# Optimization experiments

Hardware: AMD Instinct MI355X
Metric: run time of the kernel (lower is better)

The kernel has to match this reference:

```python
import jax, jax.numpy as jnp
import numpy as np

B, S, D = 8, 1024, 1152
H, HD = 16, 72  # num_heads, head_dim

def setup_inputs() -> dict:
    key = jax.random.key(0)
    ks = jax.random.split(key, 7)
    hidden_states = jax.random.normal(ks[0], (B, S, D), dtype=jnp.float32)
    cos = jax.random.uniform(ks[1], (S, HD), dtype=jnp.float32)
    sin = jax.random.uniform(ks[2], (S, HD), dtype=jnp.float32)
    qkv_w = jax.random.normal(ks[3], (3 * D, D), dtype=jnp.float32) * 0.02
    qkv_b = jnp.zeros((3 * D,), dtype=jnp.float32)
    proj_w = jax.random.normal(ks[4], (D, D), dtype=jnp.float32) * 0.02
    proj_b = jnp.zeros((D,), dtype=jnp.float32)
    return {"hidden_states": hidden_states, "cos": cos, "sin": sin,
            "qkv_w": qkv_w, "qkv_b": qkv_b, "proj_w": proj_w, "proj_b": proj_b}

def _rotate_half(x):
    x1, x2 = jnp.split(x, 2, axis=-1)
    return jnp.concatenate((-x2, x1), axis=-1)

def reference(hidden_states, cos, sin, qkv_w, qkv_b, proj_w, proj_b):
    b, s, d = hidden_states.shape
    # fused QKV projection
    qkv = hidden_states @ qkv_w.T + qkv_b            # [B,S,3D]
    qkv = qkv.reshape(b, s, 3, H, HD)
    qkv = jnp.transpose(qkv, (2, 0, 3, 1, 4))        # [3,B,H,S,HD]
    q, k, v = qkv[0], qkv[1], qkv[2]
    # rotary embedding, cos/sin broadcast [1,1,S,HD]
    c = cos[None, None, :, :]
    sn = sin[None, None, :, :]
    q = q * c + _rotate_half(q) * sn
    k = k * c + _rotate_half(k) * sn
    # SDPA
    scale = HD ** -0.5
    scores = jnp.einsum('bhqd,bhkd->bhqk', q, k) * scale
    probs = jax.nn.softmax(scores, axis=-1)
    attn = jnp.einsum('bhqk,bhkd->bhqd', probs, v)   # [B,H,S,HD]
    attn = jnp.transpose(attn, (0, 2, 1, 3)).reshape(b, s, d)
    return attn @ proj_w.T + proj_b
```

## Files before the change

kernel.cpp:

```cpp
#include <hip/hip_runtime.h>
#include <hip/hip_bf16.h>


typedef __attribute__((ext_vector_type(8))) short short8;
typedef __attribute__((ext_vector_type(4))) float f32x4;

__device__ __forceinline__ unsigned int f2bf(float f) {
    unsigned int u = __float_as_uint(f);
    return (u + 0x7FFFu + ((u >> 16) & 1u)) >> 16;
}
__device__ __forceinline__ float bf2f(unsigned short u) {
    return __uint_as_float((unsigned int)u << 16);
}

__device__ __forceinline__ void stout(float* C, size_t idx, float v) { C[idx] = v; }
__device__ __forceinline__ void stout(__hip_bfloat16* C, size_t idx, float v) {
    C[idx] = __float2bfloat16(v);
}

__device__ __forceinline__ void async_cp16(const void* g, void* l) {
    __builtin_amdgcn_global_load_lds((const __attribute__((address_space(1))) void*)g,
                                     (__attribute__((address_space(3))) void*)l, 16, 0, 0);
}

__global__ void f32_to_bf16_pair(
    const float* __restrict__ s0, unsigned short* __restrict__ d0, int n0_4,
    const float* __restrict__ s1, unsigned short* __restrict__ d1, int n1_4,
    unsigned short* __restrict__ dz, int nz_4)
{
    int i = blockIdx.x * 256 + threadIdx.x;
    if (i < n0_4) {
        float4 f = ((const float4*)s0)[i];
        ushort4 r;
        r.x = (unsigned short)f2bf(f.x);
        r.y = (unsigned short)f2bf(f.y);
        r.z = (unsigned short)f2bf(f.z);
        r.w = (unsigned short)f2bf(f.w);
        ((ushort4*)d0)[i] = r;
        return;
    }
    i -= n0_4;
    if (i < n1_4) {
        float4 f = ((const float4*)s1)[i];
        ushort4 r;
        r.x = (unsigned short)f2bf(f.x);
        r.y = (unsigned short)f2bf(f.y);
        r.z = (unsigned short)f2bf(f.z);
        r.w = (unsigned short)f2bf(f.w);
        ((ushort4*)d1)[i] = r;
        return;
    }
    i -= n1_4;
    if (i < nz_4) {
        ushort4 z; z.x = 0; z.y = 0; z.z = 0; z.w = 0;
        ((ushort4*)dz)[i] = z;
    }
}

template <int ISB, int H>
__device__ __forceinline__ void stage_ht(const unsigned short* __restrict__ g, int ldg,
                                         int k0, unsigned short* l, int w, int lane)
{
#pragma unroll
    for (int t = 0; t < 2; t++) {
        const int c  = w * 2 + t;
        const int r0 = ISB ? ((c >> 2) * 64 + H * 32 + (c & 3) * 8)
                           : ((c & 8) * 16 + H * 64 + (c & 7) * 8);
        const int rl = r0 + (lane >> 3);
        const int gg = (lane & 7) ^ (lane >> 3);
        async_cp16(g + (size_t)rl * ldg + k0 + gg * 8, l + r0 * 64);
    }
}

#define LDA(MH, SRC)                                                              \
    _Pragma("unroll") for (int mi = 0; mi < 4; ++mi) {                            \
        Af[mi][0] = *(const short8*)((SRC) + aRow + (MH) * 4096 + mi * 1024 + g0); \
        Af[mi][1] = *(const short8*)((SRC) + aRow + (MH) * 4096 + mi * 1024 + g1); \
    }

#define LDB(DST, NH, SRC)                                                         \
    _Pragma("unroll") for (int ni = 0; ni < 2; ++ni) {                            \
        DST[ni][0] = *(const short8*)((SRC) + bRow + (NH) * 2048 + ni * 1024 + g0); \
        DST[ni][1] = *(const short8*)((SRC) + bRow + (NH) * 2048 + ni * 1024 + g1); \
    }

#define MFMAS(MH, NH, PB)                                                         \
    __builtin_amdgcn_s_setprio(1);                                                \
    _Pragma("unroll") for (int mi = 0; mi < 4; ++mi)                              \
    _Pragma("unroll") for (int ni = 0; ni < 2; ++ni) {                            \
        acc[(MH) * 4 + mi][(NH) * 2 + ni] = __builtin_amdgcn_mfma_f32_16x16x32_bf16( \
            Af[mi][0], PB[ni][0], acc[(MH) * 4 + mi][(NH) * 2 + ni], 0, 0, 0);    \
        acc[(MH) * 4 + mi][(NH) * 2 + ni] = __builtin_amdgcn_mfma_f32_16x16x32_bf16( \
            Af[mi][1], PB[ni][1], acc[(MH) * 4 + mi][(NH) * 2 + ni], 0, 0, 0);    \
    }                                                                             \
    __builtin_amdgcn_s_setprio(0);

#define MIDBAR()                                                   \
    do {                                                           \
        __builtin_amdgcn_s_barrier();                              \
        asm volatile("s_waitcnt lgkmcnt(0)" ::: "memory");         \
        __builtin_amdgcn_sched_barrier(0);                         \
    } while (0)

#define ENDBAR()                                                   \
    do {                                                           \
        __builtin_amdgcn_s_barrier();                              \
        __builtin_amdgcn_sched_barrier(0);                         \
    } while (0)

template <typename OT>
__global__ __launch_bounds__(512, 2) void gemm_bt_256(
    const __hip_bfloat16* __restrict__ Abf,
    const __hip_bfloat16* __restrict__ Bbf,
    const float* __restrict__ bias,
    OT* __restrict__ C,
    int M, int Nreal, int K)
{
    __shared__ __align__(16) unsigned short smem[2][2][256 * 64];

    const int tid  = threadIdx.x;
    const int lane = tid & 63;
    const int w    = tid >> 6;
    const int wm   = w >> 2;
    const int wn   = w & 3;
    const int q    = lane >> 4;
    const int fr   = lane & 15;
    const int xr   = fr & 7;

    const int nwg = gridDim.x * gridDim.y;
    const int lin = blockIdx.y * gridDim.x + blockIdx.x;
    const int swz = (lin & 7) * (nwg >> 3) + (lin >> 3);
    const int bn  = (swz % gridDim.x) * 256;
    const int bm  = (swz / gridDim.x) * 256;

    const unsigned short* Ag = (const unsigned short*)Abf + (size_t)bm * K;
    const unsigned short* Bg = (const unsigned short*)Bbf + (size_t)bn * K;

    unsigned short* s00 = &smem[0][0][0];
    unsigned short* s01 = &smem[0][1][0];
    unsigned short* s10 = &smem[1][0][0];
    unsigned short* s11 = &smem[1][1][0];

    const int NT = K >> 6;
    const int NI = NT >> 1;

    const int aRow = (wm * 128 + fr) * 64;
    const int bRow = (wn * 64 + fr) * 64;
    const int g0   = ((0 * 4 + q) ^ xr) * 8;
    const int g1   = ((1 * 4 + q) ^ xr) * 8;

    f32x4 acc[8][4];
#pragma unroll
    for (int i = 0; i < 8; i++)
#pragma unroll
        for (int j = 0; j < 4; j++) acc[i][j] = (f32x4){0.f, 0.f, 0.f, 0.f};

    short8 Af[4][2], Bf0[2][2], Bf1[2][2];

    stage_ht<0, 0>(Ag, K, 0, s00, w, lane);
    stage_ht<0, 1>(Ag, K, 0, s00, w, lane);
    stage_ht<1, 0>(Bg, K, 0, s01, w, lane);
    stage_ht<1, 1>(Bg, K, 0, s01, w, lane);
    stage_ht<0, 0>(Ag, K, 64, s10, w, lane);
    stage_ht<1, 1>(Bg, K, 64, s10 + 16384, w, lane);
    stage_ht<0, 1>(Ag, K, 64, s10, w, lane);
    asm volatile("s_waitcnt vmcnt(6)" ::: "memory");
    ENDBAR();

#pragma unroll 1
    for (int i = 0; i < NI; i++) {
        const int k1 = (2 * i + 1) * 64;
        const int t2 = 2 * i + 2, t3 = 2 * i + 3;
        const int k2 = (t2 < NT ? t2 : NT - 1) * 64;
        const int k3 = (t3 < NT ? t3 : NT - 1) * 64;

        LDA(0, s00);
        LDB(Bf0, 0, s01);
        stage_ht<1, 0>(Bg, K, k1, s11, w, lane);
        asm volatile("s_waitcnt lgkmcnt(8)" ::: "memory");
        MIDBAR();
        MFMAS(0, 0, Bf0);
        ENDBAR();

        LDB(Bf1, 1, s01);
        stage_ht<0, 0>(Ag, K, k2, s00, w, lane);
        MIDBAR();
        MFMAS(0, 1, Bf1);
        ENDBAR();

        LDA(1, s00);
        stage_ht<1, 1>(Bg, K, k2, s01, w, lane);
        MIDBAR();
        MFMAS(1, 1, Bf1);
        ENDBAR();

        stage_ht<0, 1>(Ag, K, k2, s00, w, lane);
        asm volatile("s_waitcnt vmcnt(6)" ::: "memory");
        MIDBAR();
        MFMAS(1, 0, Bf0);
        ENDBAR();

        LDA(0, s10);
        LDB(Bf0, 0, s11);
        stage_ht<1, 0>(Bg, K, k2, s01, w, lane);
        asm volatile("s_waitcnt lgkmcnt(8)" ::: "memory");
        MIDBAR();
        MFMAS(0, 0, Bf0);
        ENDBAR();

        LDB(Bf1, 1, s11);
        stage_ht<0, 0>(Ag, K, k3, s10, w, lane);
        MIDBAR();
        MFMAS(0, 1, Bf1);
        ENDBAR();

        LDA(1, s10);
        stage_ht<1, 1>(Bg, K, k3, s11, w, lane);
        MIDBAR();
        MFMAS(1, 1, Bf1);
        ENDBAR();

        stage_ht<0, 1>(Ag, K, k3, s10, w, lane);
        asm volatile("s_waitcnt vmcnt(6)" ::: "memory");
        MIDBAR();
        MFMAS(1, 0, Bf0);
        ENDBAR();
    }

#pragma unroll
    for (int mf = 0; mf < 8; mf++) {
        const int row = bm + wm * 128 + mf * 16 + q * 4;
#pragma unroll
        for (int nf = 0; nf < 4; nf++) {
            const int col = bn + wn * 64 + nf * 16 + fr;
            if (col < Nreal) {
                const float bv = bias[col];
#pragma unroll
                for (int r = 0; r < 4; r++)
                    stout(C, (size_t)(row + r) * Nreal + col, acc[mf][nf][r] + bv);
            }
        }
    }
}

__global__ void rope_v_prep(
    const __hip_bfloat16* __restrict__ qkv,
    const float* __restrict__ cosp,
    const float* __restrict__ sinp,
    __hip_bfloat16* __restrict__ Qo,
    __hip_bfloat16* __restrict__ Ko,
    __hip_bfloat16* __restrict__ Vt)
{
    __shared__ __align__(16) unsigned short T[64 * 72];
    const int tid = threadIdx.x;
    const int bh = blockIdx.x >> 4;
    const int st = blockIdx.x & 15;
    const int b = bh >> 4, h = bh & 15;
    const size_t row0 = ((size_t)b * 1024 + st * 64) * 3456;

    const unsigned short* vsrc = (const unsigned short*)qkv + row0 + 2304 + h * 72;
#pragma unroll
    for (int k = 0; k < 3; k++) {
        const int c = tid + k * 256;
        if (c < 576) {
            const int s = c / 9, off = (c % 9) * 8;
            *(uint4*)&T[c * 8] = *(const uint4*)(vsrc + (size_t)s * 3456 + off);
        }
    }

    const unsigned short* qkvp = (const unsigned short*)qkv;
    const float QS = 0.17002324f;
#pragma unroll
    for (int k = 0; k < 3; k++) {
        const int idx = tid + k * 256;
        if (idx < 576) {
            const int sl = idx / 9, iq = idx % 9;
            const int i0 = iq * 4;
            const int sg = st * 64 + sl;
            const unsigned short* qrow = qkvp + row0 + (size_t)sl * 3456 + h * 72 + i0;

            ushort4 ql = *(const ushort4*)(qrow);
            ushort4 qh = *(const ushort4*)(qrow + 36);
            ushort4 kl = *(const ushort4*)(qrow + 1152);
            ushort4 kh = *(const ushort4*)(qrow + 1188);
            float4 cl = *(const float4*)(cosp + sg * 72 + i0);
            float4 ch = *(const float4*)(cosp + sg * 72 + i0 + 36);
            float4 nl = *(const float4*)(sinp + sg * 72 + i0);
            float4 nh = *(const float4*)(sinp + sg * 72 + i0 + 36);

            unsigned short qlv[4] = {ql.x, ql.y, ql.z, ql.w};
            unsigned short qhv[4] = {qh.x, qh.y, qh.z, qh.w};
            unsigned short klv[4] = {kl.x, kl.y, kl.z, kl.w};
            unsigned short khv[4] = {kh.x, kh.y, kh.z, kh.w};
            float clv[4] = {cl.x, cl.y, cl.z, cl.w};
            float chv[4] = {ch.x, ch.y, ch.z, ch.w};
            float nlv[4] = {nl.x, nl.y, nl.z, nl.w};
            float nhv[4] = {nh.x, nh.y, nh.z, nh.w};

            unsigned short qol[4], qoh[4], kol[4], koh[4];
#pragma unroll
            for (int j = 0; j < 4; j++) {
                const float qa = bf2f(qlv[j]), qb = bf2f(qhv[j]);
                const float ka = bf2f(klv[j]), kb = bf2f(khv[j]);
                qol[j] = (unsigned short)f2bf((qa * clv[j] - qb * nlv[j]) * QS);
                qoh[j] = (unsigned short)f2bf((qb * chv[j] + qa * nhv[j]) * QS);
                kol[j] = (unsigned short)f2bf(ka * clv[j] - kb * nlv[j]);
                koh[j] = (unsigned short)f2bf(kb * chv[j] + ka * nhv[j]);
            }
            unsigned short* qob = (unsigned short*)Qo + ((size_t)bh * 1024 + sg) * 72 + i0;
            unsigned short* kob = (unsigned short*)Ko + ((size_t)bh * 1024 + sg) * 80 + i0;
            *(ushort4*)qob        = (ushort4){qol[0], qol[1], qol[2], qol[3]};
            *(ushort4*)(qob + 36) = (ushort4){qoh[0], qoh[1], qoh[2], qoh[3]};
            *(ushort4*)kob        = (ushort4){kol[0], kol[1], kol[2], kol[3]};
            *(ushort4*)(kob + 36) = (ushort4){koh[0], koh[1], koh[2], koh[3]};
        }
    }

    __syncthreads();

    unsigned short* dst = (unsigned short*)Vt + (size_t)(bh * 16 + st) * 80 * 64;
#pragma unroll
    for (int k = 0; k < 9; k++) {
        const int o = tid + k * 256;
        const int d = o >> 5;
        const int sl = (o & 31) * 2;
        ushort2 v;
        v.x = T[sl * 72 + d];
        v.y = T[(sl + 1) * 72 + d];
        *(ushort2*)&dst[d * 64 + sl] = v;
    }
    if (tid < 64) dst[72 * 64 + tid] = (unsigned short)0x3F80;
    for (int z = tid; z < 7 * 64; z += 256) dst[73 * 64 + z] = 0;
}

__global__ __launch_bounds__(256, 4) void attn_mfma(
    const __hip_bfloat16* __restrict__ Q,
    const __hip_bfloat16* __restrict__ K,
    const __hip_bfloat16* __restrict__ Vt,
    __hip_bfloat16* __restrict__ O)
{
    __shared__ __align__(16) unsigned short Ps[4][32][72];

    const int tid  = threadIdx.x;
    const int lane = tid & 63;
    const int w    = tid >> 6;
    const int quad = lane >> 4;
    const int fr   = lane & 15;
    const int bh   = blockIdx.x & 127;
    const int qt   = blockIdx.x >> 7;
    const int qbase = qt * 128 + w * 32;

    const short8 z8 = (short8){0,0,0,0,0,0,0,0};

    const unsigned short* qp = (const unsigned short*)Q + ((size_t)bh * 1024 + qbase + fr) * 72;
    short8 qf[2][3];
#pragma unroll
    for (int sub = 0; sub < 2; sub++) {
        const unsigned short* qs = qp + sub * 16 * 72;
        qf[sub][0] = *(const short8*)(qs + quad * 8);
        qf[sub][1] = *(const short8*)(qs + 32 + quad * 8);
        qf[sub][2] = (quad == 0) ? *(const short8*)(qs + 64) : z8;
    }

    f32x4 Oa[2][5];
#pragma unroll
    for (int sub = 0; sub < 2; sub++)
#pragma unroll
        for (int n = 0; n < 5; n++) Oa[sub][n] = (f32x4){0.f, 0.f, 0.f, 0.f};

    const unsigned short* kg0 = (const unsigned short*)K + (size_t)bh * 1024 * 80;
    const unsigned short* vg0 = (const unsigned short*)Vt + (size_t)bh * 16 * 80 * 64;

#pragma unroll 1
    for (int t = 0; t < 16; t++) {
        const unsigned short* kg = kg0 + (size_t)t * 64 * 80;
        const unsigned short* vg = vg0 + (size_t)t * 80 * 64;

#pragma unroll
        for (int nt = 0; nt < 4; nt++) {
            const unsigned short* kr = kg + (nt * 16 + fr) * 80;
            short8 b0 = *(const short8*)(kr + quad * 8);
            short8 b1 = *(const short8*)(kr + 32 + quad * 8);
            short8 b2 = (quad == 0) ? *(const short8*)(kr + 64) : z8;
            f32x4 s0 = (f32x4){0.f, 0.f, 0.f, 0.f};
            f32x4 s1 = (f32x4){0.f, 0.f, 0.f, 0.f};
            __builtin_amdgcn_s_setprio(1);
            s0 = __builtin_amdgcn_mfma_f32_16x16x32_bf16(qf[0][0], b0, s0, 0, 0, 0);
            s1 = __builtin_amdgcn_mfma_f32_16x16x32_bf16(qf[1][0], b0, s1, 0, 0, 0);
            s0 = __builtin_amdgcn_mfma_f32_16x16x32_bf16(qf[0][1], b1, s0, 0, 0, 0);
            s1 = __builtin_amdgcn_mfma_f32_16x16x32_bf16(qf[1][1], b1, s1, 0, 0, 0);
            s0 = __builtin_amdgcn_mfma_f32_16x16x32_bf16(qf[0][2], b2, s0, 0, 0, 0);
            s1 = __builtin_amdgcn_mfma_f32_16x16x32_bf16(qf[1][2], b2, s1, 0, 0, 0);
            __builtin_amdgcn_s_setprio(0);
#pragma unroll
            for (int r = 0; r < 4; r++) {
                Ps[w][quad * 4 + r][nt * 16 + fr]      = (unsigned short)f2bf(exp2f(s0[r]));
                Ps[w][16 + quad * 4 + r][nt * 16 + fr] = (unsigned short)f2bf(exp2f(s1[r]));
            }
        }

#pragma unroll
        for (int ks = 0; ks < 2; ks++) {
            short8 ap0 = *(const short8*)&Ps[w][fr][ks * 32 + quad * 8];
            short8 ap1 = *(const short8*)&Ps[w][16 + fr][ks * 32 + quad * 8];
            short8 bv[5];
#pragma unroll
            for (int n = 0; n < 5; n++)
                bv[n] = *(const short8*)(vg + (n * 16 + fr) * 64 + ks * 32 + quad * 8);
            __builtin_amdgcn_s_setprio(1);
#pragma unroll
            for (int n = 0; n < 5; n++) {
                Oa[0][n] = __builtin_amdgcn_mfma_f32_16x16x32_bf16(ap0, bv[n], Oa[0][n], 0, 0, 0);
                Oa[1][n] = __builtin_amdgcn_mfma_f32_16x16x32_bf16(ap1, bv[n], Oa[1][n], 0, 0, 0);
            }
            __builtin_amdgcn_s_setprio(0);
        }
    }

    const int lsrc = (lane & 48) | 8;
    const int b = bh >> 4, h = bh & 15;
    unsigned short* ob = (unsigned short*)O;
#pragma unroll
    for (int sub = 0; sub < 2; sub++) {
        float inv[4];
#pragma unroll
        for (int r = 0; r < 4; r++)
            inv[r] = 1.f / __shfl(Oa[sub][4][r], lsrc, 64);
#pragma unroll
        for (int n = 0; n < 5; n++) {
            const int d = n * 16 + fr;
            if (d < 72) {
#pragma unroll
                for (int r = 0; r < 4; r++) {
                    const size_t idx =
                        ((size_t)b * 1024 + qbase + sub * 16 + quad * 4 + r) * 1152 + h * 72 + d;
                    ob[idx] = (unsigned short)f2bf(Oa[sub][n][r] * inv[r]);
                }
            }
        }
    }
}

extern "C" void kernel_launch(void* const* d_in, const int* in_sizes, int n_in,
                              void* d_out, int out_size, void* d_ws, size_t ws_size,
                              hipStream_t stream)
{
    const float* hs     = (const float*)d_in[0];
    const float* cosp   = (const float*)d_in[1];
    const float* sinp   = (const float*)d_in[2];
    const float* qkv_w  = (const float*)d_in[3];
    const float* qkv_b  = (const float*)d_in[4];
    const float* proj_w = (const float*)d_in[5];
    const float* proj_b = (const float*)d_in[6];
    float* out = (float*)d_out;

    char* ws = (char*)d_ws;
    __hip_bfloat16* qkv_buf = (__hip_bfloat16*)ws;
    __hip_bfloat16* Qb = (__hip_bfloat16*)(ws + 56623104);
    __hip_bfloat16* Kb = Qb + 9437184;
    __hip_bfloat16* Vt = Kb + 10485760;
    __hip_bfloat16* Ab = qkv_buf;

    unsigned short* hs_bf = (unsigned short*)Qb;
    unsigned short* qw_bf = (unsigned short*)Kb;
    unsigned short* pw_bf = (unsigned short*)Qb;

    f32_to_bf16_pair<<<13248, 256, 0, stream>>>(hs, hs_bf, 2359296,
                                                qkv_w, qw_bf, 995328,
                                                qw_bf + 3981312, 36864);
    gemm_bt_256<__hip_bfloat16>
        <<<dim3(14, 32), 512, 0, stream>>>((const __hip_bfloat16*)hs_bf,
                                           (const __hip_bfloat16*)qw_bf,
                                           qkv_b, qkv_buf, 8192, 3456, 1152);
    rope_v_prep<<<2048, 256, 0, stream>>>(qkv_buf, cosp, sinp, Qb, Kb, Vt);
    attn_mfma<<<1024, 256, 0, stream>>>(Qb, Kb, Vt, Ab);
    f32_to_bf16_pair<<<1440, 256, 0, stream>>>(proj_w, pw_bf, 331776,
                                               nullptr, nullptr, 0,
                                               pw_bf + 1327104, 36864);
    gemm_bt_256<float>
        <<<dim3(5, 32), 512, 0, stream>>>((const __hip_bfloat16*)Ab,
                                          (const __hip_bfloat16*)pw_bf,
                                          proj_b, out, 8192, 1152, 1152);
}
```

Before: 348.1 us.

## Stage K/V tiles in LDS with register-prefetched double buffering in attention

The attention kernel now cooperatively loads each 64-key K tile and V^T tile into shared memory, prefetching the next tile into registers while computing the current one, instead of every wave reading K/V straight from global memory. K and V^T are stored with a 72-element stride rather than padded to 80. The ones row and zero padding for V that produce the softmax denominator are now written once into LDS instead of global memory. This trades redundant global/L2 traffic across the four waves for two block-wide barriers per tile and extra LDS use, which may reduce occupancy.

After: 344.4 us. About the same (-1.1%).

```diff
diff --git a/kernel.cpp b/kernel.cpp
--- a/kernel.cpp
+++ b/kernel.cpp
@@ -308,7 +308,7 @@
                 koh[j] = (unsigned short)f2bf(kb * chv[j] + ka * nhv[j]);
             }
             unsigned short* qob = (unsigned short*)Qo + ((size_t)bh * 1024 + sg) * 72 + i0;
-            unsigned short* kob = (unsigned short*)Ko + ((size_t)bh * 1024 + sg) * 80 + i0;
+            unsigned short* kob = (unsigned short*)Ko + ((size_t)bh * 1024 + sg) * 72 + i0;
             *(ushort4*)qob        = (ushort4){qol[0], qol[1], qol[2], qol[3]};
             *(ushort4*)(qob + 36) = (ushort4){qoh[0], qoh[1], qoh[2], qoh[3]};
             *(ushort4*)kob        = (ushort4){kol[0], kol[1], kol[2], kol[3]};
@@ -318,7 +318,7 @@
 
     __syncthreads();
 
-    unsigned short* dst = (unsigned short*)Vt + (size_t)(bh * 16 + st) * 80 * 64;
+    unsigned short* dst = (unsigned short*)Vt + (size_t)(bh * 16 + st) * 72 * 64;
 #pragma unroll
     for (int k = 0; k < 9; k++) {
         const int o = tid + k * 256;
@@ -329,8 +329,6 @@
         v.y = T[(sl + 1) * 72 + d];
         *(ushort2*)&dst[d * 64 + sl] = v;
     }
-    if (tid < 64) dst[72 * 64 + tid] = (unsigned short)0x3F80;
-    for (int z = tid; z < 7 * 64; z += 256) dst[73 * 64 + z] = 0;
 }
 
 __global__ __launch_bounds__(256, 4) void attn_mfma(
@@ -339,6 +337,8 @@
     const __hip_bfloat16* __restrict__ Vt,
     __hip_bfloat16* __restrict__ O)
 {
+    __shared__ __align__(16) unsigned short Ks[64 * 72];
+    __shared__ __align__(16) unsigned short Vs[80][72];
     __shared__ __align__(16) unsigned short Ps[4][32][72];
 
     const int tid  = threadIdx.x;
@@ -352,6 +352,9 @@
 
     const short8 z8 = (short8){0,0,0,0,0,0,0,0};
 
+    for (int idx = tid; idx < 8 * 72; idx += 256)
+        Vs[72 + idx / 72][idx % 72] = (idx < 72) ? (unsigned short)0x3F80 : (unsigned short)0;
+
     const unsigned short* qp = (const unsigned short*)Q + ((size_t)bh * 1024 + qbase + fr) * 72;
     short8 qf[2][3];
 #pragma unroll
@@ -368,17 +371,46 @@
 #pragma unroll
         for (int n = 0; n < 5; n++) Oa[sub][n] = (f32x4){0.f, 0.f, 0.f, 0.f};
 
-    const unsigned short* kg0 = (const unsigned short*)K + (size_t)bh * 1024 * 80;
-    const unsigned short* vg0 = (const unsigned short*)Vt + (size_t)bh * 16 * 80 * 64;
+    const unsigned short* kg0 = (const unsigned short*)K + (size_t)bh * 1024 * 72;
+    const unsigned short* vg0 = (const unsigned short*)Vt + (size_t)bh * 16 * 72 * 64;
+
+    const unsigned short* gsrc[5];
+    unsigned short* ldst[5];
+#pragma unroll
+    for (int c = 0; c < 5; c++) {
+        const int g = tid + c * 256;
+        if (g < 576) {
+            gsrc[c] = kg0 + g * 8;
+            ldst[c] = &Ks[g * 8];
+        } else {
+            const int v = (g - 576) & 1023;
+            gsrc[c] = vg0 + (size_t)v * 8;
+            ldst[c] = &Vs[v >> 3][(v & 7) * 8];
+        }
+    }
+    const bool five = (tid < 128);
+
+    uint4 stg[5];
+#pragma unroll
+    for (int c = 0; c < 4; c++) stg[c] = *(const uint4*)(gsrc[c]);
+    if (five) stg[4] = *(const uint4*)(gsrc[4]);
+#pragma unroll
+    for (int c = 0; c < 4; c++) *(uint4*)ldst[c] = stg[c];
+    if (five) *(uint4*)ldst[4] = stg[4];
+    __syncthreads();
 
 #pragma unroll 1
     for (int t = 0; t < 16; t++) {
-        const unsigned short* kg = kg0 + (size_t)t * 64 * 80;
-        const unsigned short* vg = vg0 + (size_t)t * 80 * 64;
+        if (t < 15) {
+            const size_t off = (size_t)(t + 1) * 4608;
+#pragma unroll
+            for (int c = 0; c < 4; c++) stg[c] = *(const uint4*)(gsrc[c] + off);
+            if (five) stg[4] = *(const uint4*)(gsrc[4] + off);
+        }
 
 #pragma unroll
         for (int nt = 0; nt < 4; nt++) {
-            const unsigned short* kr = kg + (nt * 16 + fr) * 80;
+            const unsigned short* kr = &Ks[(nt * 16 + fr) * 72];
             short8 b0 = *(const short8*)(kr + quad * 8);
             short8 b1 = *(const short8*)(kr + 32 + quad * 8);
             short8 b2 = (quad == 0) ? *(const short8*)(kr + 64) : z8;
@@ -403,17 +435,22 @@
         for (int ks = 0; ks < 2; ks++) {
             short8 ap0 = *(const short8*)&Ps[w][fr][ks * 32 + quad * 8];
             short8 ap1 = *(const short8*)&Ps[w][16 + fr][ks * 32 + quad * 8];
-            short8 bv[5];
-#pragma unroll
-            for (int n = 0; n < 5; n++)
-                bv[n] = *(const short8*)(vg + (n * 16 + fr) * 64 + ks * 32 + quad * 8);
-            __builtin_amdgcn_s_setprio(1);
 #pragma unroll
             for (int n = 0; n < 5; n++) {
-                Oa[0][n] = __builtin_amdgcn_mfma_f32_16x16x32_bf16(ap0, bv[n], Oa[0][n], 0, 0, 0);
-                Oa[1][n] = __builtin_amdgcn_mfma_f32_16x16x32_bf16(ap1, bv[n], Oa[1][n], 0, 0, 0);
+                short8 bv = *(const short8*)&Vs[n * 16 + fr][ks * 32 + quad * 8];
+                __builtin_amdgcn_s_setprio(1);
+                Oa[0][n] = __builtin_amdgcn_mfma_f32_16x16x32_bf16(ap0, bv, Oa[0][n], 0, 0, 0);
+                Oa[1][n] = __builtin_amdgcn_mfma_f32_16x16x32_bf16(ap1, bv, Oa[1][n], 0, 0, 0);
+                __builtin_amdgcn_s_setprio(0);
             }
-            __builtin_amdgcn_s_setprio(0);
+        }
+
+        if (t < 15) {
+            __syncthreads();
+#pragma unroll
+            for (int c = 0; c < 4; c++) *(uint4*)ldst[c] = stg[c];
+            if (five) *(uint4*)ldst[4] = stg[4];
+            __syncthreads();
         }
     }
 
@@ -458,7 +495,7 @@
     __hip_bfloat16* qkv_buf = (__hip_bfloat16*)ws;
     __hip_bfloat16* Qb = (__hip_bfloat16*)(ws + 56623104);
     __hip_bfloat16* Kb = Qb + 9437184;
-    __hip_bfloat16* Vt = Kb + 10485760;
+    __hip_bfloat16* Vt = Kb + 9437184;
     __hip_bfloat16* Ab = qkv_buf;
 
     unsigned short* hs_bf = (unsigned short*)Qb;
```

## Stage K/V tiles in LDS with double-buffered async copies in attention

Applied to the files above, without the earlier changes.

The attention kernel now copies each 64-key K tile and V^T tile into shared memory with global_load_lds, double-buffered and prefetched two tiles ahead, instead of reading K and V straight from global memory in every wave. The K and V^T layouts shrink from a padding of 80 to 72 columns. V^T uses an XOR swizzle to avoid LDS bank conflicts, and the ones/zero padding rows used for the softmax row-sum move to a small shared constant buffer. The aim is to cut redundant global and L2 traffic across the four waves and overlap loads with MFMA work. In exchange, launch bounds drop to 2 blocks per CU because of the larger LDS use, and block barriers are added each iteration.

Result: faster. 320.5 us (-7.9%).

```diff
diff --git a/kernel.cpp b/kernel.cpp
--- a/kernel.cpp
+++ b/kernel.cpp
@@ -308,7 +308,7 @@
                 koh[j] = (unsigned short)f2bf(kb * chv[j] + ka * nhv[j]);
             }
             unsigned short* qob = (unsigned short*)Qo + ((size_t)bh * 1024 + sg) * 72 + i0;
-            unsigned short* kob = (unsigned short*)Ko + ((size_t)bh * 1024 + sg) * 80 + i0;
+            unsigned short* kob = (unsigned short*)Ko + ((size_t)bh * 1024 + sg) * 72 + i0;
             *(ushort4*)qob        = (ushort4){qol[0], qol[1], qol[2], qol[3]};
             *(ushort4*)(qob + 36) = (ushort4){qoh[0], qoh[1], qoh[2], qoh[3]};
             *(ushort4*)kob        = (ushort4){kol[0], kol[1], kol[2], kol[3]};
@@ -318,7 +318,7 @@
 
     __syncthreads();
 
-    unsigned short* dst = (unsigned short*)Vt + (size_t)(bh * 16 + st) * 80 * 64;
+    unsigned short* dst = (unsigned short*)Vt + (size_t)(bh * 16 + st) * 72 * 64;
 #pragma unroll
     for (int k = 0; k < 9; k++) {
         const int o = tid + k * 256;
@@ -327,18 +327,37 @@
         ushort2 v;
         v.x = T[sl * 72 + d];
         v.y = T[(sl + 1) * 72 + d];
-        *(ushort2*)&dst[d * 64 + sl] = v;
-    }
-    if (tid < 64) dst[72 * 64 + tid] = (unsigned short)0x3F80;
-    for (int z = tid; z < 7 * 64; z += 256) dst[73 * 64 + z] = 0;
-}
-
-__global__ __launch_bounds__(256, 4) void attn_mfma(
+        const int col = ((((sl >> 3) ^ (d & 7)) << 3)) + (sl & 7);
+        *(ushort2*)&dst[d * 64 + col] = v;
+    }
+}
+
+__device__ __forceinline__ void attn_stage(const unsigned short* kt, const unsigned short* vt,
+                                           unsigned short* kl, unsigned short* vl,
+                                           int w, int lane)
+{
+#pragma unroll
+    for (int c = 0; c < 5; c++) {
+        const int call = w + c * 4;
+        if (call < 18) {
+            const bool isv = (call >= 9);
+            const int o = (isv ? call - 9 : call) * 512;
+            const unsigned short* s = (isv ? vt : kt) + o + lane * 8;
+            unsigned short* d = (isv ? vl : kl) + o;
+            async_cp16(s, d);
+        }
+    }
+}
+
+__global__ __launch_bounds__(256, 2) void attn_mfma(
     const __hip_bfloat16* __restrict__ Q,
     const __hip_bfloat16* __restrict__ K,
     const __hip_bfloat16* __restrict__ Vt,
     __hip_bfloat16* __restrict__ O)
 {
+    __shared__ __align__(16) unsigned short KsA[2][64 * 72];
+    __shared__ __align__(16) unsigned short VsA[2][72 * 64];
+    __shared__ __align__(16) unsigned short Vones[8 * 64];
     __shared__ __align__(16) unsigned short Ps[4][32][72];
 
     const int tid  = threadIdx.x;
@@ -352,6 +371,9 @@
 
     const short8 z8 = (short8){0,0,0,0,0,0,0,0};
 
+    for (int idx = tid; idx < 512; idx += 256)
+        Vones[idx] = (idx < 64) ? (unsigned short)0x3F80 : (unsigned short)0;
+
     const unsigned short* qp = (const unsigned short*)Q + ((size_t)bh * 1024 + qbase + fr) * 72;
     short8 qf[2][3];
 #pragma unroll
@@ -368,17 +390,30 @@
 #pragma unroll
         for (int n = 0; n < 5; n++) Oa[sub][n] = (f32x4){0.f, 0.f, 0.f, 0.f};
 
-    const unsigned short* kg0 = (const unsigned short*)K + (size_t)bh * 1024 * 80;
-    const unsigned short* vg0 = (const unsigned short*)Vt + (size_t)bh * 16 * 80 * 64;
+    const unsigned short* kg0 = (const unsigned short*)K + (size_t)bh * 1024 * 72;
+    const unsigned short* vg0 = (const unsigned short*)Vt + (size_t)bh * 16 * 72 * 64;
+
+    attn_stage(kg0,        vg0,        &KsA[0][0], &VsA[0][0], w, lane);
+    attn_stage(kg0 + 4608, vg0 + 4608, &KsA[1][0], &VsA[1][0], w, lane);
+    __builtin_amdgcn_sched_barrier(0);
 
 #pragma unroll 1
     for (int t = 0; t < 16; t++) {
-        const unsigned short* kg = kg0 + (size_t)t * 64 * 80;
-        const unsigned short* vg = vg0 + (size_t)t * 80 * 64;
+        if (t < 15) {
+            if (w < 2) asm volatile("s_waitcnt vmcnt(5)" ::: "memory");
+            else       asm volatile("s_waitcnt vmcnt(4)" ::: "memory");
+        } else {
+            asm volatile("s_waitcnt vmcnt(0)" ::: "memory");
+        }
+        __builtin_amdgcn_sched_barrier(0);
+        __builtin_amdgcn_s_barrier();
+
+        const unsigned short* kb = (t & 1) ? &KsA[1][0] : &KsA[0][0];
+        const unsigned short* vb = (t & 1) ? &VsA[1][0] : &VsA[0][0];
 
 #pragma unroll
         for (int nt = 0; nt < 4; nt++) {
-            const unsigned short* kr = kg + (nt * 16 + fr) * 80;
+            const unsigned short* kr = kb + (nt * 16 + fr) * 72;
             short8 b0 = *(const short8*)(kr + quad * 8);
             short8 b1 = *(const short8*)(kr + 32 + quad * 8);
             short8 b2 = (quad == 0) ? *(const short8*)(kr + 64) : z8;
@@ -403,17 +438,30 @@
         for (int ks = 0; ks < 2; ks++) {
             short8 ap0 = *(const short8*)&Ps[w][fr][ks * 32 + quad * 8];
             short8 ap1 = *(const short8*)&Ps[w][16 + fr][ks * 32 + quad * 8];
-            short8 bv[5];
-#pragma unroll
-            for (int n = 0; n < 5; n++)
-                bv[n] = *(const short8*)(vg + (n * 16 + fr) * 64 + ks * 32 + quad * 8);
-            __builtin_amdgcn_s_setprio(1);
+            const int jx8 = ((ks * 4 + quad) ^ (fr & 7)) * 8;
 #pragma unroll
             for (int n = 0; n < 5; n++) {
-                Oa[0][n] = __builtin_amdgcn_mfma_f32_16x16x32_bf16(ap0, bv[n], Oa[0][n], 0, 0, 0);
-                Oa[1][n] = __builtin_amdgcn_mfma_f32_16x16x32_bf16(ap1, bv[n], Oa[1][n], 0, 0, 0);
+                const unsigned short* p =
+                    (n < 4) ? (vb + (n * 16 + fr) * 64 + jx8)
+                            : ((fr < 8) ? (vb + (64 + fr) * 64 + jx8)
+                                        : (&Vones[0] + (fr - 8) * 64 + jx8));
+                short8 bv = *(const short8*)p;
+                __builtin_amdgcn_s_setprio(1);
+                Oa[0][n] = __builtin_amdgcn_mfma_f32_16x16x32_bf16(ap0, bv, Oa[0][n], 0, 0, 0);
+                Oa[1][n] = __builtin_amdgcn_mfma_f32_16x16x32_bf16(ap1, bv, Oa[1][n], 0, 0, 0);
+                __builtin_amdgcn_s_setprio(0);
             }
-            __builtin_amdgcn_s_setprio(0);
+        }
+
+        __builtin_amdgcn_s_barrier();
+        __builtin_amdgcn_sched_barrier(0);
+
+        if (t < 14) {
+            unsigned short* kd = (t & 1) ? &KsA[1][0] : &KsA[0][0];
+            unsigned short* vd = (t & 1) ? &VsA[1][0] : &VsA[0][0];
+            attn_stage(kg0 + (size_t)(t + 2) * 4608, vg0 + (size_t)(t + 2) * 4608,
+                       kd, vd, w, lane);
+            __builtin_amdgcn_sched_barrier(0);
         }
     }
 
@@ -458,7 +506,7 @@
     __hip_bfloat16* qkv_buf = (__hip_bfloat16*)ws;
     __hip_bfloat16* Qb = (__hip_bfloat16*)(ws + 56623104);
     __hip_bfloat16* Kb = Qb + 9437184;
-    __hip_bfloat16* Vt = Kb + 10485760;
+    __hip_bfloat16* Vt = Kb + 9437184;
     __hip_bfloat16* Ab = qkv_buf;
 
     unsigned short* hs_bf = (unsigned short*)Qb;
```
